# Optimization experiments

Hardware: AMD Instinct MI355X
Metric: run time of the kernel (lower is better)

## Reference

```python
import jax, jax.numpy as jnp
import numpy as np

K = 5        # spline kernel_size per dim (dim=2 -> 25 kernel weights)
NPG = 75     # MNIST superpixel nodes per graph


def _spline_conv(x, src, dst, pseudo, emask, W, root, bias):
    """SplineConv, dim=2, kernel_size=5, degree=1 open splines, aggr='mean'.
    emask in {0,1} masks out coalesced-away (duplicate/self-loop) edges."""
    n = x.shape[0]
    v = jnp.clip(pseudo, 0.0, 1.0) * (K - 1)
    bot = jnp.clip(jnp.floor(v), 0, K - 2)
    frac = v - bot                                   # [E,2]
    bot = bot.astype(jnp.int32)
    xj = x[src] * emask[:, None]                     # [E,Fin] gathered source feats
    # aggregate-then-transform: acc[k,i,:] = sum over edges into i with basis k
    acc = jnp.zeros((K * K, n, x.shape[1]), x.dtype)
    for o0 in (0, 1):
        for o1 in (0, 1):
            w = (frac[:, 0] if o0 else 1.0 - frac[:, 0]) * (frac[:, 1] if o1 else 1.0 - frac[:, 1])
            kk = (bot[:, 0] + o0) + K * (bot[:, 1] + o1)
            acc = acc.at[kk, dst].add(w[:, None] * xj)
    out = jnp.einsum('knf,kfo->no', acc, W)
    deg = jax.ops.segment_sum(emask, dst, num_segments=n)
    return out / jnp.maximum(deg, 1.0)[:, None] + x @ root + bias


def _pool(x, pos, valid, batch, src, dst, emask, size, G, B):
    """voxel_grid + max_pool with static shapes: S=B*G*G clusters, masked."""
    S = B * G * G
    c = jnp.clip(jnp.floor(pos / size).astype(jnp.int32), 0, G - 1)
    cl = batch * (G * G) + c[:, 1] * G + c[:, 0]
    xm = jnp.where(valid[:, None] > 0, x, -1e30)
    px = jax.ops.segment_max(xm, cl, num_segments=S)
    cnt = jax.ops.segment_sum(valid, cl, num_segments=S)
    sval = (cnt > 0).astype(x.dtype)
    px = jnp.where(sval[:, None] > 0, px, 0.0)
    ppos = jax.ops.segment_sum(pos * valid[:, None], cl, num_segments=S) / jnp.maximum(cnt, 1.0)[:, None]
    nb = jnp.arange(S, dtype=jnp.int32) // (G * G)
    # remap edges to clusters; mask self loops and duplicates (= coalesce)
    nsrc, ndst = cl[src], cl[dst]
    m = (emask > 0) & (nsrc != ndst)
    a0 = jnp.where(m, nsrc, S)
    b0 = jnp.where(m, ndst, S)
    order = jnp.lexsort((b0, a0))
    a, b = a0[order], b0[order]
    first = jnp.concatenate([jnp.array([True]), (a[1:] != a[:-1]) | (b[1:] != b[:-1])])
    keep = jnp.zeros(src.shape[0], dtype=bool).at[order].set(first & (a < S))
    kf = keep.astype(x.dtype)
    # T.Cartesian(cat=False, norm=True): pseudo = (pos_src-pos_dst)/(2*max|.|)+0.5
    cart = ppos[nsrc] - ppos[ndst]
    amax = jnp.maximum(jnp.max(jnp.abs(cart) * kf[:, None]), 1e-12)
    pseudo = cart / (2.0 * amax) + 0.5
    return px, ppos, sval, nb, nsrc, ndst, kf, pseudo


def _forward(x, pos, src, dst, W1, r1, b1, W2, r2, b2, W3, r3, b3, fw1, fb1, fw2, fb2):
    N = x.shape[0]
    B = N // NPG
    batch = jnp.arange(N, dtype=jnp.int32) // NPG
    valid = jnp.ones((N,), x.dtype)
    emask = jnp.ones((src.shape[0],), x.dtype)
    cart = pos[src] - pos[dst]
    pseudo = cart / (2.0 * jnp.maximum(jnp.max(jnp.abs(cart)), 1e-12)) + 0.5
    x = jax.nn.elu(_spline_conv(x, src, dst, pseudo, emask, W1, r1, b1))
    x, pos, valid, batch, src, dst, emask, pseudo = _pool(x, pos, valid, batch, src, dst, emask, 5.0, 6, B)
    x = jax.nn.elu(_spline_conv(x, src, dst, pseudo, emask, W2, r2, b2))
    x, pos, valid, batch, src, dst, emask, pseudo = _pool(x, pos, valid, batch, src, dst, emask, 7.0, 5, B)
    x = jax.nn.elu(_spline_conv(x, src, dst, pseudo, emask, W3, r3, b3))
    # max_pool_x(cluster, x, batch, size=4): 2x2 voxel grid (size=14, end=27.99)
    c = jnp.clip(jnp.floor(pos / 14.0).astype(jnp.int32), 0, 1)
    cl = batch * 4 + c[:, 1] * 2 + c[:, 0]
    xm = jnp.where(valid[:, None] > 0, x, -1e30)
    px = jax.ops.segment_max(xm, cl, num_segments=B * 4)
    cnt = jax.ops.segment_sum(valid, cl, num_segments=B * 4)
    px = jnp.where((cnt > 0)[:, None], px, 0.0)
    h = jax.nn.elu(px.reshape(B, 4 * 64) @ fw1.T + fb1)
    logits = h @ fw2.T + fb2  # F.dropout is identity in eval mode
    return jax.nn.log_softmax(logits, axis=1)


def setup_inputs() -> dict:
    key = jax.random.key(0)
    ks = jax.random.split(key, 16)
    B, EPG = 1024, 1392
    N = B * NPG
    x = jax.random.normal(ks[0], (N, 1), jnp.float32)
    pos = jax.random.uniform(ks[1], (N, 2), jnp.float32) * 27.99
    s = jax.random.randint(ks[2], (B, EPG), 0, NPG)
    d = (s + 1 + jax.random.randint(ks[3], (B, EPG), 0, NPG - 1)) % NPG  # no self loops
    off = (jnp.arange(B, dtype=jnp.int32) * NPG)[:, None]
    src = (s + off).reshape(-1)
    dst = (d + off).reshape(-1)
    rn = lambda k, sh, sc: jax.random.normal(k, sh, jnp.float32) * sc
    return dict(x=x, pos=pos, src=src, dst=dst,
                W1=rn(ks[4], (25, 1, 32), 0.2), r1=rn(ks[5], (1, 32), 0.2), b1=jnp.zeros((32,), jnp.float32),
                W2=rn(ks[6], (25, 32, 64), 0.05), r2=rn(ks[7], (32, 64), 0.1), b2=jnp.zeros((64,), jnp.float32),
                W3=rn(ks[8], (25, 64, 64), 0.04), r3=rn(ks[9], (64, 64), 0.08), b3=jnp.zeros((64,), jnp.float32),
                fw1=rn(ks[10], (128, 256), 0.06), fb1=jnp.zeros((128,), jnp.float32),
                fw2=rn(ks[11], (10, 128), 0.09), fb2=jnp.zeros((10,), jnp.float32))


def reference(x, pos, src, dst, W1, r1, b1, W2, r2, b2, W3, r3, b3, fw1, fb1, fw2, fb2):
    return _forward(x, pos, src, dst, W1, r1, b1, W2, r2, b2, W3, r3, b3, fw1, fb1, fw2, fb2)
```

## Files before the change

kernel.cpp:

```cpp
#include <hip/hip_runtime.h>
#include <math.h>

#define NPG 75
#define KDIM 5

typedef _Float16 half8 __attribute__((ext_vector_type(8)));
typedef float f32x4 __attribute__((ext_vector_type(4)));

__device__ __forceinline__ float eluf(float v){ return v > 0.f ? v : expf(v) - 1.f; }

__device__ __forceinline__ void atomAddF(float* p, float v){ unsafeAtomicAdd(p, v); }

__device__ __forceinline__ unsigned fenc(float f){
    unsigned u = __float_as_uint(f);
    return (u & 0x80000000u) ? ~u : (u | 0x80000000u);
}
__device__ __forceinline__ float fdec(unsigned u){
    return (u & 0x80000000u) ? __uint_as_float(u & 0x7FFFFFFFu) : __uint_as_float(~u);
}

__device__ __forceinline__ void fma25(float (&r)[25], const float (&wx)[5], const float (&wyx)[5]){
    #pragma unroll
    for (int b1 = 0; b1 < 5; b1++)
        #pragma unroll
        for (int b0 = 0; b0 < 5; b0++)
            asm("v_fmac_f32 %0, %1, %2" : "+v"(r[b1 * 5 + b0]) : "v"(wx[b0]), "v"(wyx[b1]));
}

__device__ __forceinline__ void spline2(float c0, float c1, float am, int* kks, float* wsp){
    float denom = 2.f * fmaxf(am, 1e-12f);
    float p0 = c0 / denom + 0.5f;
    float p1 = c1 / denom + 0.5f;
    p0 = fminf(fmaxf(p0, 0.f), 1.f) * 4.f;
    p1 = fminf(fmaxf(p1, 0.f), 1.f) * 4.f;
    float b0 = fminf(floorf(p0), 3.f);
    float b1 = fminf(floorf(p1), 3.f);
    float f0 = p0 - b0, f1 = p1 - b1;
    int i0 = (int)b0, i1 = (int)b1;
    wsp[0] = (1.f - f0) * (1.f - f1); kks[0] = i0     + KDIM *  i1;
    wsp[1] =        f0  * (1.f - f1); kks[1] = i0 + 1 + KDIM *  i1;
    wsp[2] = (1.f - f0) *        f1 ; kks[2] = i0     + KDIM * (i1 + 1);
    wsp[3] =        f0  *        f1 ; kks[3] = i0 + 1 + KDIM * (i1 + 1);
}

__device__ __forceinline__ void spline_pay(float2 c, float denom, float* d){
    float p0 = fminf(fmaxf(c.x / denom + 0.5f, 0.f), 1.f) * 4.f;
    float p1 = fminf(fmaxf(c.y / denom + 0.5f, 0.f), 1.f) * 4.f;
    float b0 = fminf(floorf(p0), 3.f);
    float b1 = fminf(floorf(p1), 3.f);
    int i0 = (int)b0, i1 = (int)b1;
    float f0 = p0 - b0, f1 = p1 - b1;
    #pragma unroll
    for (int k = 0; k < 4; k++){
        d[k]     = (k == i0) ? (1.f - f0) : ((k == i0 + 1) ? f0 : 0.f);
        d[4 + k] = (k == i1) ? (1.f - f1) : ((k == i1 + 1) ? f1 : 0.f);
    }
}

__global__ __launch_bounds__(256) void prep_k(
        const float* __restrict__ W2, const float* __restrict__ r2,
        const float* __restrict__ W3, const float* __restrict__ r3,
        _Float16* __restrict__ Wz2, _Float16* __restrict__ Wz3, int nW,
        const float* __restrict__ pos, const int* __restrict__ src,
        const int* __restrict__ dst, int E4, int gA, unsigned* __restrict__ outbits){
    const int blk = blockIdx.x;
    if (blk < nW){
        int gid = blk * 256 + threadIdx.x;
        const int T2 = 26 * 32 * 64;
        const int T3 = 26 * 64 * 64;
        const float* W; const float* root; _Float16* Wz; int FIN; int g;
        if (gid < T2){ W = W2; root = r2; Wz = Wz2; FIN = 32; g = gid; }
        else if (gid < T2 + T3){ W = W3; root = r3; Wz = Wz3; FIN = 64; g = gid - T2; }
        else return;
        int k = g >> 6, n = g & 63;
        float v = (k < 25 * FIN) ? W[(size_t)k * 64 + n] : root[(size_t)(k - 25 * FIN) * 64 + n];
        int kt = k >> 5, kr = k & 31, quad = kr >> 3, j = kr & 7;
        int lane = (quad << 4) | (n & 15);
        int nt = n >> 4;
        Wz[(((size_t)(kt * 4 + nt) * 64 + lane) << 3) + j] = (_Float16)v;
    } else {
        float cand = 0.f;
        for (int i = (blk - nW) * 256 + threadIdx.x; i < E4; i += gA * 256){
            int4 s4 = ((const int4*)src)[i];
            int4 d4 = ((const int4*)dst)[i];
            #pragma unroll
            for (int k = 0; k < 4; k++){
                int s = (&s4.x)[k], d = (&d4.x)[k];
                float c0 = pos[s*2]   - pos[d*2];
                float c1 = pos[s*2+1] - pos[d*2+1];
                cand = fmaxf(cand, fmaxf(fabsf(c0), fabsf(c1)));
            }
        }
        __shared__ float sm[256];
        sm[threadIdx.x] = cand; __syncthreads();
        for (int o = 128; o > 0; o >>= 1){
            if (threadIdx.x < o) sm[threadIdx.x] = fmaxf(sm[threadIdx.x], sm[threadIdx.x + o]);
            __syncthreads();
        }
        if (threadIdx.x == 0) atomicMax(outbits, __float_as_uint(sm[0]));
    }
}

__global__ __launch_bounds__(512) void conv1dedup_k(
        const float* __restrict__ x, const float* __restrict__ pos,
        const int* __restrict__ src, const int* __restrict__ dst, int EPG,
        const unsigned* __restrict__ amaxp,
        const float* __restrict__ W1, const float* __restrict__ r1, const float* __restrict__ b1,
        float* __restrict__ px1, float* __restrict__ pp1, float* __restrict__ sv1,
        int* __restrict__ easrc, float2* __restrict__ ecart,
        int* __restrict__ rowptr2, int* __restrict__ kcnt, unsigned* __restrict__ amaxbits){
    __shared__ __align__(16) float acc[NPG * 28];
    __shared__ float deg[NPG];
    __shared__ float xl[NPG], p0l[NPG], p1l[NPG];
    __shared__ int   cli[NPG];
    __shared__ float W1s[800], r1s[32], b1s[32];
    __shared__ unsigned px[36 * 32];
    __shared__ float cnt[36], ps[72], ppS[72];
    __shared__ unsigned pm[36 * 36];
    __shared__ float degs[36];
    __shared__ int rs[37], cur[36];
    __shared__ float red[8];
    __shared__ unsigned short sdS[2048];

    const int b = blockIdx.x, t = threadIdx.x;
    const int lane = t & 63, wid = t >> 6;
    const int n0 = b * NPG, e0 = b * EPG;

    const float am = __uint_as_float(*amaxp);

    for (int i = t; i < NPG * 28; i += 512) acc[i] = 0.f;
    for (int i = t; i < 36 * 32; i += 512) px[i] = 0u;
    for (int i = t; i < 36 * 36; i += 512) pm[i] = 0xFFFFFFFFu;
    if (t < NPG) deg[t] = 0.f;
    if (t < 36){ cnt[t] = 0.f; degs[t] = 0.f; }
    if (t < 72) ps[t] = 0.f;
    for (int i = t; i < 800; i += 512) W1s[i] = W1[i];
    if (t < 32){ r1s[t] = r1[t]; b1s[t] = b1[t]; }
    if (t < NPG){
        float p0 = pos[(n0 + t) * 2], p1 = pos[(n0 + t) * 2 + 1];
        xl[t] = x[n0 + t]; p0l[t] = p0; p1l[t] = p1;
        int c0 = min(max((int)floorf(p0 / 5.f), 0), 5);
        int c1 = min(max((int)floorf(p1 / 5.f), 0), 5);
        cli[t] = c1 * 6 + c0;
    }
    __syncthreads();

    if (t < NPG){
        int c = cli[t];
        atomAddF(&cnt[c], 1.f);
        atomAddF(&ps[c*2],     p0l[t]);
        atomAddF(&ps[c*2 + 1], p1l[t]);
    }
    #pragma unroll 4
    for (int it = 0; it < 4; it++){
        int e = t + it * 512;
        if (e < EPG){
            int s = src[e0 + e] - n0;
            int d = dst[e0 + e] - n0;
            sdS[e] = (unsigned short)(s | (d << 8));
            float c0 = p0l[s] - p0l[d];
            float c1 = p1l[s] - p1l[d];
            int kks[4]; float wsp[4];
            spline2(c0, c1, am, kks, wsp);
            float xv = xl[s];
            #pragma unroll
            for (int c = 0; c < 4; c++) atomAddF(&acc[d*28 + kks[c]], wsp[c] * xv);
            atomAddF(&deg[d], 1.f);
        }
    }
    __syncthreads();

    if (t < 36){
        float c = cnt[t], m = fmaxf(c, 1.f);
        float q0 = ps[t*2] / m, q1 = ps[t*2 + 1] / m;
        ppS[t*2] = q0; ppS[t*2 + 1] = q1;
        pp1[(b*36 + t)*2]     = q0;
        pp1[(b*36 + t)*2 + 1] = q1;
        sv1[b*36 + t] = (c > 0.f) ? 1.f : 0.f;
    }
    {
        const int o = t & 31;
        float wreg[25];
        #pragma unroll
        for (int k = 0; k < 25; k++) wreg[k] = W1s[k * 32 + o];
        const float rro = r1s[o], bbo = b1s[o];
        const int ii = t >> 5;
        #pragma unroll
        for (int r = 0; r < 5; r++){
            int i = ii + r * 16;
            if (i < NPG){
                const float4* ar = (const float4*)(acc + i * 28);
                float s = 0.f;
                #pragma unroll
                for (int q = 0; q < 7; q++){
                    float4 aq = ar[q];
                    s += aq.x * wreg[q*4];
                    if (q*4 + 1 < 25) s += aq.y * wreg[q*4 + 1];
                    if (q*4 + 2 < 25) s += aq.z * wreg[q*4 + 2];
                    if (q*4 + 3 < 25) s += aq.w * wreg[q*4 + 3];
                }
                float v = s / fmaxf(deg[i], 1.f) + xl[i] * rro + bbo;
                v = eluf(v);
                atomicMax(&px[cli[i]*32 + o], fenc(v));
            }
        }
    }
    int lab[4];
    #pragma unroll 4
    for (int it = 0; it < 4; it++){
        int e = t + it * 512;
        lab[it] = 0;
        if (e < EPG){
            int sd = (int)sdS[e];
            int a  = cli[sd & 255];
            int bb = cli[sd >> 8];
            lab[it] = a | (bb << 8) | ((a != bb) ? 0x10000 : 0);
            if (a != bb) atomicMin(&pm[a * 36 + bb], (unsigned)e);
        }
    }
    __syncthreads();

    for (int idx = t; idx < 36 * 32; idx += 512){
        int s_ = idx >> 5;
        px1[(size_t)(b*36)*32 + idx] = (cnt[s_] > 0.f) ? fdec(px[idx]) : 0.f;
    }
    float cand = 0.f;
    unsigned keptM = 0;
    #pragma unroll 4
    for (int it = 0; it < 4; it++){
        int e = t + it * 512;
        int L = lab[it];
        if (L & 0x10000){
            int a = L & 255, bb = (L >> 8) & 255;
            if (pm[a * 36 + bb] == (unsigned)e){
                keptM |= 1u << it;
                atomAddF(&degs[bb], 1.f);
                float c0 = ppS[a*2]     - ppS[bb*2];
                float c1 = ppS[a*2 + 1] - ppS[bb*2 + 1];
                cand = fmaxf(cand, fmaxf(fabsf(c0), fabsf(c1)));
            }
        }
    }
    #pragma unroll
    for (int o = 1; o < 64; o <<= 1) cand = fmaxf(cand, __shfl_xor(cand, o, 64));
    if (lane == 0) red[wid] = cand;
    __syncthreads();
    if (t == 0){
        float m = red[0];
        #pragma unroll
        for (int i = 1; i < 8; i++) m = fmaxf(m, red[i]);
        atomicMax(amaxbits, __float_as_uint(m));
    }
    if (t < 64){
        int v = (t < 36) ? (int)degs[t] : 0;
        int incl = v;
        #pragma unroll
        for (int o = 1; o < 64; o <<= 1){
            int u = __shfl_up(incl, o, 64);
            if (t >= o) incl += u;
        }
        if (t == 0) rs[0] = 0;
        if (t < 36) rs[t + 1] = incl;
    }
    __syncthreads();
    if (t < 36){
        rowptr2[(b*36 + t)*2]     = e0 + rs[t];
        rowptr2[(b*36 + t)*2 + 1] = e0 + rs[t + 1];
        cur[t] = rs[t];
    }
    if (t == 0) kcnt[b] = rs[36];
    __syncthreads();
    #pragma unroll 4
    for (int it = 0; it < 4; it++){
        if (keptM & (1u << it)){
            int L = lab[it];
            int a = L & 255, bb = (L >> 8) & 255;
            int slot = atomicAdd(&cur[bb], 1);
            easrc[e0 + slot] = b*36 + a;
            ecart[e0 + slot] = make_float2(ppS[a*2] - ppS[bb*2], ppS[a*2 + 1] - ppS[bb*2 + 1]);
        }
    }
}

__global__ __launch_bounds__(1024) void dedup_pool_k(
        const int* __restrict__ easrc_in, const int* __restrict__ rowptr_in,
        const int* __restrict__ kcnt_in,
        const float* __restrict__ xin,
        const float* __restrict__ pp1, const float* __restrict__ sv1,
        int EPG,
        float* __restrict__ px2, float* __restrict__ pp2, float* __restrict__ sv2,
        int* __restrict__ easrc, float2* __restrict__ ecart,
        int* __restrict__ rowptr2, int* __restrict__ kcnt, unsigned* __restrict__ amaxbits){
    constexpr int GG = 25, NN = 36;
    __shared__ unsigned pm[GG * GG];
    __shared__ float degs[GG];
    __shared__ int rs[GG + 1];
    __shared__ int cur[GG];
    __shared__ float red[16];
    __shared__ int   clS[NN];
    __shared__ int   vld[NN];
    __shared__ int   rsS[NN + 1];
    __shared__ float ppS[2 * GG];
    __shared__ unsigned px[GG * 64];
    __shared__ float cnt[GG], ps[2 * GG];
    __shared__ unsigned short abS[1280];

    const int b = blockIdx.x, t = threadIdx.x;
    const int lane = t & 63, wid = t >> 6;
    const int e0 = b * EPG;
    const int cb25 = b * GG;
    const int nb36 = b * NN;

    for (int i = t; i < GG * GG; i += 1024) pm[i] = 0xFFFFFFFFu;
    for (int i = t; i < GG * 64; i += 1024) px[i] = 0u;
    if (t < GG){ degs[t] = 0.f; cnt[t] = 0.f; }
    if (t < 2 * GG) ps[t] = 0.f;
    if (t < NN){
        float v  = sv1[nb36 + t];
        float p0 = pp1[(nb36 + t)*2], p1 = pp1[(nb36 + t)*2 + 1];
        int c0 = min(max((int)floorf(p0 / 7.f), 0), 4);
        int c1 = min(max((int)floorf(p1 / 7.f), 0), 4);
        clS[t] = c1 * 5 + c0;
        vld[t] = (v > 0.f) ? 1 : 0;
        rsS[t] = rowptr_in[(nb36 + t)*2] - e0;
    }
    if (t == 0) rsS[NN] = kcnt_in[b];
    __syncthreads();

    const int kn = rsS[NN];

    if (t < NN && vld[t]){
        int c = clS[t];
        atomAddF(&cnt[c], 1.f);
        atomAddF(&ps[c*2],     pp1[(nb36 + t)*2]);
        atomAddF(&ps[c*2 + 1], pp1[(nb36 + t)*2 + 1]);
    }
    for (int idx = t; idx < NN * 64; idx += 1024){
        int i = idx >> 6, f = idx & 63;
        if (vld[i])
            atomicMax(&px[clS[i]*64 + f], fenc(xin[(size_t)(nb36 + i)*64 + f]));
    }
    #pragma unroll 2
    for (int it = 0; it < 2; it++){
        int s = t + it * 1024;
        if (s < kn){
            int r = 0;
            while (r < NN - 1 && rsS[r + 1] <= s) r++;
            int a2 = clS[easrc_in[e0 + s] - nb36];
            int b2 = clS[r];
            abS[s] = (unsigned short)(a2 | (b2 << 8) | ((a2 != b2) ? 0x8000 : 0));
            if (a2 != b2) atomicMin(&pm[a2 * GG + b2], (unsigned)s);
        }
    }
    __syncthreads();

    if (t < GG){
        float c = cnt[t], m = fmaxf(c, 1.f);
        float q0 = ps[t*2] / m, q1 = ps[t*2 + 1] / m;
        ppS[t*2] = q0; ppS[t*2 + 1] = q1;
        pp2[(cb25 + t)*2]     = q0;
        pp2[(cb25 + t)*2 + 1] = q1;
        sv2[cb25 + t] = (c > 0.f) ? 1.f : 0.f;
    }
    for (int idx = t; idx < GG * 64; idx += 1024){
        int s_ = idx >> 6;
        px2[(size_t)cb25*64 + idx] = (cnt[s_] > 0.f) ? fdec(px[idx]) : 0.f;
    }
    __syncthreads();

    float cand = 0.f;
    #pragma unroll 2
    for (int it = 0; it < 2; it++){
        int s = t + it * 1024;
        if (s < kn){
            int A = (int)abS[s];
            if (A & 0x8000){
                int a2 = A & 255, b2 = (A >> 8) & 127;
                if (pm[a2 * GG + b2] == (unsigned)s){
                    atomAddF(&degs[b2], 1.f);
                    float c0 = ppS[a2*2]     - ppS[b2*2];
                    float c1 = ppS[a2*2 + 1] - ppS[b2*2 + 1];
                    cand = fmaxf(cand, fmaxf(fabsf(c0), fabsf(c1)));
                }
            }
        }
    }
    #pragma unroll
    for (int o = 1; o < 64; o <<= 1) cand = fmaxf(cand, __shfl_xor(cand, o, 64));
    if (lane == 0) red[wid] = cand;
    __syncthreads();
    if (t == 0){
        float m = red[0];
        #pragma unroll
        for (int i = 1; i < 16; i++) m = fmaxf(m, red[i]);
        atomicMax(amaxbits, __float_as_uint(m));
    }
    if (t < 64){
        int v = (t < GG) ? (int)degs[t] : 0;
        int incl = v;
        #pragma unroll
        for (int o = 1; o < 64; o <<= 1){
            int u = __shfl_up(incl, o, 64);
            if (t >= o) incl += u;
        }
        if (t == 0) rs[0] = 0;
        if (t < GG) rs[t + 1] = incl;
    }
    __syncthreads();
    if (t < GG){
        rowptr2[(cb25 + t)*2]     = e0 + rs[t];
        rowptr2[(cb25 + t)*2 + 1] = e0 + rs[t + 1];
        cur[t] = rs[t];
    }
    if (t == 0) kcnt[b] = rs[GG];
    __syncthreads();
    #pragma unroll 2
    for (int it = 0; it < 2; it++){
        int s = t + it * 1024;
        if (s < kn){
            int A = (int)abS[s];
            if (A & 0x8000){
                int a2 = A & 255, b2 = (A >> 8) & 127;
                if (pm[a2 * GG + b2] == (unsigned)s){
                    int slot = atomicAdd(&cur[b2], 1);
                    easrc[e0 + slot] = cb25 + a2;
                    ecart[e0 + slot] = make_float2(ppS[a2*2] - ppS[b2*2], ppS[a2*2 + 1] - ppS[b2*2 + 1]);
                }
            }
        }
    }
}

__global__ __launch_bounds__(256) void conv_gather32_k(
        const float* __restrict__ x, const int* __restrict__ easrc,
        const float2* __restrict__ ecart, const unsigned* __restrict__ amaxp,
        const int* __restrict__ rowptr2, _Float16* __restrict__ Aout){
    constexpr int FIN = 32;
    constexpr int KTOT = 26 * FIN;
    __shared__ __align__(16) float pay[4][36][8];
    __shared__ int asrcS[4][36];
    const int w = threadIdx.x >> 6, lane = threadIdx.x & 63;
    const int node = blockIdx.x * 4 + w;
    const int row0 = rowptr2[node*2], row1 = rowptr2[node*2 + 1];
    const int ne = row1 - row0;
    const int sub = lane >> 5;
    const int f = lane & (FIN - 1);

    if (lane < ne){
        float am = __uint_as_float(*amaxp);
        spline_pay(ecart[row0 + lane], 2.f * fmaxf(am, 1e-12f), &pay[w][lane][0]);
        asrcS[w][lane] = easrc[row0 + lane];
    }

    float r[25];
    #pragma unroll
    for (int b = 0; b < 25; b++) r[b] = 0.f;

    int j = sub;
    int aNext = 0;
    float xvCur = 0.f;
    if (j < ne){
        int aCur = asrcS[w][j];
        xvCur = x[(size_t)aCur * FIN + f];
        int j1 = (j + 2 < ne) ? j + 2 : j;
        aNext = asrcS[w][j1];
    }
    for (; j < ne; j += 2){
        int jN  = j + 2;
        int jNs = (jN < ne) ? jN : j;
        int jN2 = (jN + 2 < ne) ? jN + 2 : jNs;
        float xvN = x[(size_t)aNext * FIN + f];
        int aN2 = asrcS[w][jN2];
        float4 wa = *(const float4*)&pay[w][j][0];
        float4 wb = *(const float4*)&pay[w][j][4];
        float wx4 = 1.f - (wa.x + wa.y + wa.z + wa.w);
        float wy4 = 1.f - (wb.x + wb.y + wb.z + wb.w);
        float wx[5]  = {wa.x, wa.y, wa.z, wa.w, wx4};
        float wyx[5] = {wb.x * xvCur, wb.y * xvCur, wb.z * xvCur, wb.w * xvCur, wy4 * xvCur};
        fma25(r, wx, wyx);
        xvCur = xvN; aNext = aN2;
    }

    #pragma unroll
    for (int b = 0; b < 25; b++) r[b] += __shfl_xor(r[b], 32, 64);

    float inv = 1.f / (float)max(ne, 1);
    _Float16* dstrow = Aout + (size_t)node * KTOT;
    #pragma unroll
    for (int b = 0; b < 25; b++)
        if ((b & 1) == sub) dstrow[b * 32 + f] = (_Float16)(r[b] * inv);
    if (sub == 0) dstrow[25 * 32 + f] = (_Float16)x[(size_t)node * 32 + f];
}

__global__ __launch_bounds__(256) void conv_mfma832_k(
        const _Float16* __restrict__ A, const _Float16* __restrict__ Wz,
        const float* __restrict__ bias, int M, float* __restrict__ out){
    constexpr int KTOT = 832;
    constexpr int NSTEP = KTOT / 32;
    const int w = threadIdx.x >> 6, lane = threadIdx.x & 63;
    const int m0 = blockIdx.x * 64 + w * 16;
    const int quad = lane >> 4;

    f32x4 acc[4];
    #pragma unroll
    for (int nt = 0; nt < 4; nt++) acc[nt] = (f32x4){0.f, 0.f, 0.f, 0.f};

    const half8* __restrict__ Arow = (const half8*)(A + (size_t)(m0 + (lane & 15)) * KTOT);
    const half8* __restrict__ Wp   = (const half8*)Wz + lane;

    for (int kt = 0; kt < NSTEP; kt++){
        half8 a = Arow[kt * 4 + quad];
        #pragma unroll
        for (int nt = 0; nt < 4; nt++){
            half8 b = Wp[(kt * 4 + nt) * 64];
            acc[nt] = __builtin_amdgcn_mfma_f32_16x16x32_f16(a, b, acc[nt], 0, 0, 0);
        }
    }

    float* cp = out + (size_t)m0 * 64;
    const int r = quad * 4, c = lane & 15;
    #pragma unroll
    for (int nt = 0; nt < 4; nt++){
        float bv = bias[nt * 16 + c];
        #pragma unroll
        for (int i = 0; i < 4; i++)
            cp[(size_t)(r + i) * 64 + nt * 16 + c] = eluf(acc[nt][i] + bv);
    }
}

__global__ __launch_bounds__(1024) void conv3pf_k(
        const float* __restrict__ x,
        const int* __restrict__ easrc, const float2* __restrict__ ecart,
        const unsigned* __restrict__ amaxp,
        const int* __restrict__ rowptr3,
        const _Float16* __restrict__ Wz, const float* __restrict__ bias,
        const float* __restrict__ pp2, const float* __restrict__ sv2,
        const float* __restrict__ fw1, const float* __restrict__ fb1,
        const float* __restrict__ fw2, const float* __restrict__ fb2,
        float* __restrict__ out){
    constexpr int PAD = 1672;
    __shared__ __align__(16) _Float16 Alds[32 * PAD];
    __shared__ __align__(16) float scr[4096];
    __shared__ int asrcS[16][24];
    __shared__ unsigned px4[4 * 64];
    __shared__ float cnt4[4];
    __shared__ int cli25[25];
    __shared__ float xr[256];
    __shared__ float h[128];
    __shared__ float lg[10];
    __shared__ float lse;

    const int b = blockIdx.x, t = threadIdx.x;
    const int w = t >> 6, lane = t & 63;
    const int cb25 = b * 25;

    {
        unsigned* az = (unsigned*)&Alds[25 * PAD];
        for (int i = t; i < 7 * PAD / 2; i += 1024) az[i] = 0u;
    }
    if (t < 256) px4[t] = 0u;
    if (t < 4) cnt4[t] = 0.f;
    if (t < 25){
        float v = sv2[cb25 + t];
        float p0 = pp2[(cb25 + t)*2], p1 = pp2[(cb25 + t)*2 + 1];
        int c0 = min(max((int)floorf(p0 / 14.f), 0), 1);
        int c1 = min(max((int)floorf(p1 / 14.f), 0), 1);
        cli25[t] = (v > 0.f) ? (c1 * 2 + c0) : -1;
    }

    const float am = __uint_as_float(*amaxp);
    const float denom = 2.f * fmaxf(am, 1e-12f);
    float* payW = scr + w * 192;

    #pragma unroll
    for (int i = 0; i < 2; i++){
        const int nloc = w * 2 + i;
        if (nloc < 25){
            const int node = cb25 + nloc;
            const int row0 = rowptr3[node*2], row1 = rowptr3[node*2 + 1];
            const int ne = row1 - row0;

            if (lane < ne){
                spline_pay(ecart[row0 + lane], denom, payW + lane * 8);
                asrcS[w][lane] = easrc[row0 + lane];
            }

            float r[25];
            #pragma unroll
            for (int bq = 0; bq < 25; bq++) r[bq] = 0.f;

            int j = 0;
            int aNext = 0;
            float xvCur = 0.f;
            if (j < ne){
                int aCur = asrcS[w][j];
                xvCur = x[(size_t)aCur * 64 + lane];
                int j1 = (1 < ne) ? 1 : 0;
                aNext = asrcS[w][j1];
            }
            for (; j < ne; j++){
                int jN  = j + 1;
                int jNs = (jN < ne) ? jN : j;
                int jN2 = (jN + 1 < ne) ? jN + 1 : jNs;
                float xvN = x[(size_t)aNext * 64 + lane];
                int aN2 = asrcS[w][jN2];
                float4 wa = *(const float4*)(payW + j * 8);
                float4 wb = *(const float4*)(payW + j * 8 + 4);
                float wx4 = 1.f - (wa.x + wa.y + wa.z + wa.w);
                float wy4 = 1.f - (wb.x + wb.y + wb.z + wb.w);
                float wx[5]  = {wa.x, wa.y, wa.z, wa.w, wx4};
                float wyx[5] = {wb.x * xvCur, wb.y * xvCur, wb.z * xvCur, wb.w * xvCur, wy4 * xvCur};
                fma25(r, wx, wyx);
                xvCur = xvN; aNext = aN2;
            }

            float inv = 1.f / (float)max(ne, 1);
            _Float16* dstrow = &Alds[nloc * PAD];
            #pragma unroll
            for (int bq = 0; bq < 25; bq++) dstrow[bq * 64 + lane] = (_Float16)(r[bq] * inv);
            dstrow[25 * 64 + lane] = (_Float16)x[(size_t)node * 64 + lane];
        }
    }
    __syncthreads();

    if (t < 25 && cli25[t] >= 0) atomAddF(&cnt4[cli25[t]], 1.f);

    float* Cpart = scr;
    float* out3L = scr + 2048;

    const int tile = w & 7, khalf = w >> 3;
    const int mt = tile >> 2, nt = tile & 3;
    const int quad = lane >> 4, mr = lane & 15;
    f32x4 acc = (f32x4){0.f, 0.f, 0.f, 0.f};
    const _Float16* arow = &Alds[(mt * 16 + mr) * PAD];
    const half8* __restrict__ Wp = (const half8*)Wz + lane;
    const int kt0 = khalf * 26;
    for (int kt = 0; kt < 26; kt++){
        half8 a = *(const half8*)(arow + (kt0 + kt) * 32 + quad * 8);
        half8 bb = Wp[((kt0 + kt) * 4 + nt) * 64];
        acc = __builtin_amdgcn_mfma_f32_16x16x32_f16(a, bb, acc, 0, 0, 0);
    }
    const int r_ = quad * 4, c_ = lane & 15;
    if (khalf == 1){
        float* Cp = Cpart + tile * 256;
        #pragma unroll
        for (int i = 0; i < 4; i++) Cp[(r_ + i) * 16 + c_] = acc[i];
    }
    __syncthreads();
    if (khalf == 0){
        const float* Cp = Cpart + tile * 256;
        float bv = bias[nt * 16 + c_];
        #pragma unroll
        for (int i = 0; i < 4; i++)
            out3L[(mt * 16 + r_ + i) * 64 + nt * 16 + c_] = eluf(acc[i] + Cp[(r_ + i) * 16 + c_] + bv);
    }
    __syncthreads();

    for (int idx = t; idx < 25 * 64; idx += 1024){
        int i = idx >> 6, f = idx & 63;
        if (cli25[i] >= 0)
            atomicMax(&px4[cli25[i]*64 + f], fenc(out3L[i * 64 + f]));
    }
    __syncthreads();
    if (t < 256) xr[t] = (cnt4[t >> 6] > 0.f) ? fdec(px4[t]) : 0.f;
    __syncthreads();
    if (t < 128){
        float s = fb1[t];
        const float4* wrow = (const float4*)(fw1 + (size_t)t * 256);
        #pragma unroll 4
        for (int i = 0; i < 64; i++){
            float4 q = wrow[i];
            s += xr[i*4]   * q.x;
            s += xr[i*4+1] * q.y;
            s += xr[i*4+2] * q.z;
            s += xr[i*4+3] * q.w;
        }
        h[t] = eluf(s);
    }
    __syncthreads();
    if (t < 10){
        float s2 = fb2[t];
        const float* w2 = fw2 + (size_t)t * 128;
        for (int j = 0; j < 128; j++) s2 += h[j] * w2[j];
        lg[t] = s2;
    }
    __syncthreads();
    if (t == 0){
        float m = lg[0];
        for (int c = 1; c < 10; c++) m = fmaxf(m, lg[c]);
        float se = 0.f;
        for (int c = 0; c < 10; c++) se += expf(lg[c] - m);
        lse = m + logf(se);
    }
    __syncthreads();
    if (t < 10) out[(size_t)b*10 + t] = lg[t] - lse;
}

extern "C" void kernel_launch(void* const* d_in, const int* in_sizes, int n_in,
                              void* d_out, int out_size, void* d_ws, size_t ws_size,
                              hipStream_t stream) {
    const float* x   = (const float*)d_in[0];
    const float* pos = (const float*)d_in[1];
    const int*   src = (const int*)d_in[2];
    const int*   dst = (const int*)d_in[3];
    const float* W1  = (const float*)d_in[4];
    const float* r1  = (const float*)d_in[5];
    const float* b1  = (const float*)d_in[6];
    const float* W2  = (const float*)d_in[7];
    const float* r2  = (const float*)d_in[8];
    const float* b2  = (const float*)d_in[9];
    const float* W3  = (const float*)d_in[10];
    const float* r3  = (const float*)d_in[11];
    const float* b3  = (const float*)d_in[12];
    const float* fw1 = (const float*)d_in[13];
    const float* fb1 = (const float*)d_in[14];
    const float* fw2 = (const float*)d_in[15];
    const float* fb2 = (const float*)d_in[16];
    float* out = (float*)d_out;

    const int N   = in_sizes[0];
    const int E   = in_sizes[2];
    const int B   = N / NPG;
    const int EPG = E / B;
    const int S1  = B * 36;
    const int S2  = B * 25;

    float* w = (float*)d_ws;
    size_t off = 0;
    auto alloc = [&](size_t nelem){ size_t o = off; off += (nelem + 63) & ~(size_t)63; return o; };

    size_t o_scal = alloc(4);
    size_t o_px1  = alloc((size_t)S1 * 32);
    size_t o_pp1  = alloc((size_t)S1 * 2);
    size_t o_sv1  = alloc(S1);
    size_t o_easrc= alloc(E);
    size_t o_ecart= alloc((size_t)2 * E);
    size_t o_kcnt = alloc(B);
    size_t o_rp2  = alloc((size_t)2 * S1);
    size_t o_rp3  = alloc((size_t)2 * S2);
    size_t o_out2 = alloc((size_t)S1 * 64);
    size_t o_px2  = alloc((size_t)S2 * 64);
    size_t o_pp2  = alloc((size_t)S2 * 2);
    size_t o_sv2  = alloc(S2);
    size_t o_wz2  = alloc((size_t)26 * 32 * 64 / 2 + 64);
    size_t o_wz3  = alloc((size_t)26 * 64 * 64 / 2 + 64);
    size_t o_accA = alloc(((size_t)S1 * 832 + 1) / 2);

    hipMemsetAsync(w + o_scal, 0, 4 * sizeof(float), stream);

    unsigned* scal = (unsigned*)(w + o_scal);
    _Float16* Wz2  = (_Float16*)(w + o_wz2);
    _Float16* Wz3  = (_Float16*)(w + o_wz3);
    _Float16* A16  = (_Float16*)(w + o_accA);

    const int E4 = E / 4;
    int gA = (E4 + 255) / 256; if (gA > 512) gA = 512;
    const int nW = (26 * 32 * 64 + 26 * 64 * 64 + 255) / 256;
    prep_k<<<nW + gA, 256, 0, stream>>>(W2, r2, W3, r3, Wz2, Wz3, nW,
                                        pos, src, dst, E4, gA, scal + 0);

    conv1dedup_k<<<B, 512, 0, stream>>>(x, pos, src, dst, EPG, scal + 0, W1, r1, b1,
                                        w + o_px1, w + o_pp1, w + o_sv1,
                                        (int*)(w + o_easrc), (float2*)(w + o_ecart),
                                        (int*)(w + o_rp2), (int*)(w + o_kcnt), scal + 1);

    conv_gather32_k<<<S1 / 4, 256, 0, stream>>>(
        w + o_px1, (int*)(w + o_easrc), (const float2*)(w + o_ecart), scal + 1,
        (int*)(w + o_rp2), A16);
    conv_mfma832_k<<<S1 / 64, 256, 0, stream>>>(A16, Wz2, b2, S1, w + o_out2);

    dedup_pool_k<<<B, 1024, 0, stream>>>(
        (int*)(w + o_easrc), (int*)(w + o_rp2), (int*)(w + o_kcnt),
        w + o_out2, w + o_pp1, w + o_sv1, EPG,
        w + o_px2, w + o_pp2, w + o_sv2,
        (int*)(w + o_easrc), (float2*)(w + o_ecart),
        (int*)(w + o_rp3), (int*)(w + o_kcnt), scal + 2);

    conv3pf_k<<<B, 1024, 0, stream>>>(
        w + o_px2,
        (int*)(w + o_easrc), (const float2*)(w + o_ecart), scal + 2,
        (int*)(w + o_rp3), Wz3, b3,
        w + o_pp2, w + o_sv2,
        fw1, fb1, fw2, fb2, out);
}
```

Baseline: 320.1 us.

## Fuse conv2 MFMA GEMM into per-graph dedup/pool kernel, dropping out2 buffer

Merges the conv2 MFMA GEMM into the dedup/voxel-pool kernel, giving one 256-thread block per graph. Each graph's 36 cluster rows are multiplied in 16-row tiles, and the ELU output is max-reduced straight into shared pooled features through atomicMax, so the out2 intermediate is never written to or read from global memory. This removes a kernel launch and the global round trip. In exchange, the dedup block shrinks from 1024 to 256 threads and some MFMA work is wasted on padded rows (36 rows spread over 48), which may lower parallelism per graph.

```diff
diff --git a/kernel.cpp b/kernel.cpp
--- a/kernel.cpp
+++ b/kernel.cpp
@@ -282,155 +282,6 @@
     }
 }
 
-__global__ __launch_bounds__(1024) void dedup_pool_k(
-        const int* __restrict__ easrc_in, const int* __restrict__ rowptr_in,
-        const int* __restrict__ kcnt_in,
-        const float* __restrict__ xin,
-        const float* __restrict__ pp1, const float* __restrict__ sv1,
-        int EPG,
-        float* __restrict__ px2, float* __restrict__ pp2, float* __restrict__ sv2,
-        int* __restrict__ easrc, float2* __restrict__ ecart,
-        int* __restrict__ rowptr2, int* __restrict__ kcnt, unsigned* __restrict__ amaxbits){
-    constexpr int GG = 25, NN = 36;
-    __shared__ unsigned pm[GG * GG];
-    __shared__ float degs[GG];
-    __shared__ int rs[GG + 1];
-    __shared__ int cur[GG];
-    __shared__ float red[16];
-    __shared__ int   clS[NN];
-    __shared__ int   vld[NN];
-    __shared__ int   rsS[NN + 1];
-    __shared__ float ppS[2 * GG];
-    __shared__ unsigned px[GG * 64];
-    __shared__ float cnt[GG], ps[2 * GG];
-    __shared__ unsigned short abS[1280];
-
-    const int b = blockIdx.x, t = threadIdx.x;
-    const int lane = t & 63, wid = t >> 6;
-    const int e0 = b * EPG;
-    const int cb25 = b * GG;
-    const int nb36 = b * NN;
-
-    for (int i = t; i < GG * GG; i += 1024) pm[i] = 0xFFFFFFFFu;
-    for (int i = t; i < GG * 64; i += 1024) px[i] = 0u;
-    if (t < GG){ degs[t] = 0.f; cnt[t] = 0.f; }
-    if (t < 2 * GG) ps[t] = 0.f;
-    if (t < NN){
-        float v  = sv1[nb36 + t];
-        float p0 = pp1[(nb36 + t)*2], p1 = pp1[(nb36 + t)*2 + 1];
-        int c0 = min(max((int)floorf(p0 / 7.f), 0), 4);
-        int c1 = min(max((int)floorf(p1 / 7.f), 0), 4);
-        clS[t] = c1 * 5 + c0;
-        vld[t] = (v > 0.f) ? 1 : 0;
-        rsS[t] = rowptr_in[(nb36 + t)*2] - e0;
-    }
-    if (t == 0) rsS[NN] = kcnt_in[b];
-    __syncthreads();
-
-    const int kn = rsS[NN];
-
-    if (t < NN && vld[t]){
-        int c = clS[t];
-        atomAddF(&cnt[c], 1.f);
-        atomAddF(&ps[c*2],     pp1[(nb36 + t)*2]);
-        atomAddF(&ps[c*2 + 1], pp1[(nb36 + t)*2 + 1]);
-    }
-    for (int idx = t; idx < NN * 64; idx += 1024){
-        int i = idx >> 6, f = idx & 63;
-        if (vld[i])
-            atomicMax(&px[clS[i]*64 + f], fenc(xin[(size_t)(nb36 + i)*64 + f]));
-    }
-    #pragma unroll 2
-    for (int it = 0; it < 2; it++){
-        int s = t + it * 1024;
-        if (s < kn){
-            int r = 0;
-            while (r < NN - 1 && rsS[r + 1] <= s) r++;
-            int a2 = clS[easrc_in[e0 + s] - nb36];
-            int b2 = clS[r];
-            abS[s] = (unsigned short)(a2 | (b2 << 8) | ((a2 != b2) ? 0x8000 : 0));
-            if (a2 != b2) atomicMin(&pm[a2 * GG + b2], (unsigned)s);
-        }
-    }
-    __syncthreads();
-
-    if (t < GG){
-        float c = cnt[t], m = fmaxf(c, 1.f);
-        float q0 = ps[t*2] / m, q1 = ps[t*2 + 1] / m;
-        ppS[t*2] = q0; ppS[t*2 + 1] = q1;
-        pp2[(cb25 + t)*2]     = q0;
-        pp2[(cb25 + t)*2 + 1] = q1;
-        sv2[cb25 + t] = (c > 0.f) ? 1.f : 0.f;
-    }
-    for (int idx = t; idx < GG * 64; idx += 1024){
-        int s_ = idx >> 6;
-        px2[(size_t)cb25*64 + idx] = (cnt[s_] > 0.f) ? fdec(px[idx]) : 0.f;
-    }
-    __syncthreads();
-
-    float cand = 0.f;
-    #pragma unroll 2
-    for (int it = 0; it < 2; it++){
-        int s = t + it * 1024;
-        if (s < kn){
-            int A = (int)abS[s];
-            if (A & 0x8000){
-                int a2 = A & 255, b2 = (A >> 8) & 127;
-                if (pm[a2 * GG + b2] == (unsigned)s){
-                    atomAddF(&degs[b2], 1.f);
-                    float c0 = ppS[a2*2]     - ppS[b2*2];
-                    float c1 = ppS[a2*2 + 1] - ppS[b2*2 + 1];
-                    cand = fmaxf(cand, fmaxf(fabsf(c0), fabsf(c1)));
-                }
-            }
-        }
-    }
-    #pragma unroll
-    for (int o = 1; o < 64; o <<= 1) cand = fmaxf(cand, __shfl_xor(cand, o, 64));
-    if (lane == 0) red[wid] = cand;
-    __syncthreads();
-    if (t == 0){
-        float m = red[0];
-        #pragma unroll
-        for (int i = 1; i < 16; i++) m = fmaxf(m, red[i]);
-        atomicMax(amaxbits, __float_as_uint(m));
-    }
-    if (t < 64){
-        int v = (t < GG) ? (int)degs[t] : 0;
-        int incl = v;
-        #pragma unroll
-        for (int o = 1; o < 64; o <<= 1){
-            int u = __shfl_up(incl, o, 64);
-            if (t >= o) incl += u;
-        }
-        if (t == 0) rs[0] = 0;
-        if (t < GG) rs[t + 1] = incl;
-    }
-    __syncthreads();
-    if (t < GG){
-        rowptr2[(cb25 + t)*2]     = e0 + rs[t];
-        rowptr2[(cb25 + t)*2 + 1] = e0 + rs[t + 1];
-        cur[t] = rs[t];
-    }
-    if (t == 0) kcnt[b] = rs[GG];
-    __syncthreads();
-    #pragma unroll 2
-    for (int it = 0; it < 2; it++){
-        int s = t + it * 1024;
-        if (s < kn){
-            int A = (int)abS[s];
-            if (A & 0x8000){
-                int a2 = A & 255, b2 = (A >> 8) & 127;
-                if (pm[a2 * GG + b2] == (unsigned)s){
-                    int slot = atomicAdd(&cur[b2], 1);
-                    easrc[e0 + slot] = cb25 + a2;
-                    ecart[e0 + slot] = make_float2(ppS[a2*2] - ppS[b2*2], ppS[a2*2 + 1] - ppS[b2*2 + 1]);
-                }
-            }
-        }
-    }
-}
-
 __global__ __launch_bounds__(256) void conv_gather32_k(
         const float* __restrict__ x, const int* __restrict__ easrc,
         const float2* __restrict__ ecart, const unsigned* __restrict__ amaxp,
@@ -492,39 +343,176 @@
     if (sub == 0) dstrow[25 * 32 + f] = (_Float16)x[(size_t)node * 32 + f];
 }
 
-__global__ __launch_bounds__(256) void conv_mfma832_k(
+__global__ __launch_bounds__(256) void mfma2pool_k(
         const _Float16* __restrict__ A, const _Float16* __restrict__ Wz,
-        const float* __restrict__ bias, int M, float* __restrict__ out){
-    constexpr int KTOT = 832;
-    constexpr int NSTEP = KTOT / 32;
-    const int w = threadIdx.x >> 6, lane = threadIdx.x & 63;
-    const int m0 = blockIdx.x * 64 + w * 16;
-    const int quad = lane >> 4;
-
-    f32x4 acc[4];
+        const float* __restrict__ bias,
+        const int* __restrict__ easrc_in, const int* __restrict__ rowptr_in,
+        const int* __restrict__ kcnt_in,
+        const float* __restrict__ pp1, const float* __restrict__ sv1,
+        int EPG,
+        float* __restrict__ px2, float* __restrict__ pp2, float* __restrict__ sv2,
+        int* __restrict__ easrc, float2* __restrict__ ecart,
+        int* __restrict__ rowptr3, int* __restrict__ kcnt, unsigned* __restrict__ amaxbits){
+    constexpr int GG = 25, NN = 36;
+    __shared__ unsigned pm[GG * GG];
+    __shared__ float degs[GG];
+    __shared__ int rs[GG + 1];
+    __shared__ int cur[GG];
+    __shared__ float red[4];
+    __shared__ int   clS[NN];
+    __shared__ int   vld[NN];
+    __shared__ int   rsS[NN + 1];
+    __shared__ float ppS[2 * GG];
+    __shared__ unsigned px[GG * 64];
+    __shared__ float cnt[GG], ps[2 * GG];
+    __shared__ unsigned short abS[1280];
+
+    const int b = blockIdx.x, t = threadIdx.x;
+    const int w = t >> 6, lane = t & 63;
+    const int e0 = b * EPG;
+    const int cb25 = b * GG;
+    const int nb36 = b * NN;
+
+    for (int i = t; i < GG * GG; i += 256) pm[i] = 0xFFFFFFFFu;
+    for (int i = t; i < GG * 64; i += 256) px[i] = 0u;
+    if (t < GG){ degs[t] = 0.f; cnt[t] = 0.f; }
+    if (t < 2 * GG) ps[t] = 0.f;
+    if (t < NN){
+        float v  = sv1[nb36 + t];
+        float p0 = pp1[(nb36 + t)*2], p1 = pp1[(nb36 + t)*2 + 1];
+        int c0 = min(max((int)floorf(p0 / 7.f), 0), 4);
+        int c1 = min(max((int)floorf(p1 / 7.f), 0), 4);
+        clS[t] = c1 * 5 + c0;
+        vld[t] = (v > 0.f) ? 1 : 0;
+        rsS[t] = rowptr_in[(nb36 + t)*2] - e0;
+    }
+    if (t == 0) rsS[NN] = kcnt_in[b];
+    __syncthreads();
+
+    const int kn = rsS[NN];
+
+    if (t < NN && vld[t]){
+        int c = clS[t];
+        atomAddF(&cnt[c], 1.f);
+        atomAddF(&ps[c*2],     pp1[(nb36 + t)*2]);
+        atomAddF(&ps[c*2 + 1], pp1[(nb36 + t)*2 + 1]);
+    }
+    #pragma unroll 6
+    for (int it = 0; it < 6; it++){
+        int s = t + it * 256;
+        if (s < kn){
+            int r = 0;
+            while (r < NN - 1 && rsS[r + 1] <= s) r++;
+            int a2 = clS[easrc_in[e0 + s] - nb36];
+            int b2 = clS[r];
+            abS[s] = (unsigned short)(a2 | (b2 << 8) | ((a2 != b2) ? 0x8000 : 0));
+            if (a2 != b2) atomicMin(&pm[a2 * GG + b2], (unsigned)s);
+        }
+    }
+    {
+        const int quad = lane >> 4, c_ = lane & 15;
+        const half8* __restrict__ Wp = (const half8*)Wz + lane;
+        #pragma unroll
+        for (int tt = 0; tt < 3; tt++){
+            const int tile = w + tt * 4;
+            const int mt = tile >> 2, nt = tile & 3;
+            const int row_l = mt * 16 + c_;
+            const bool rok = (row_l < NN);
+            const half8* Arow = rok ? (const half8*)(A + (size_t)(nb36 + row_l) * 832) : (const half8*)A;
+            f32x4 acc = (f32x4){0.f, 0.f, 0.f, 0.f};
+            for (int kt = 0; kt < 26; kt++){
+                half8 a = rok ? Arow[kt * 4 + quad] : (half8){};
+                half8 bb = Wp[(kt * 4 + nt) * 64];
+                acc = __builtin_amdgcn_mfma_f32_16x16x32_f16(a, bb, acc, 0, 0, 0);
+            }
+            const int r_ = quad * 4;
+            float bv = bias[nt * 16 + c_];
+            #pragma unroll
+            for (int i = 0; i < 4; i++){
+                int rowp = mt * 16 + r_ + i;
+                if (rowp < NN && vld[rowp]){
+                    float v = eluf(acc[i] + bv);
+                    atomicMax(&px[clS[rowp]*64 + nt * 16 + c_], fenc(v));
+                }
+            }
+        }
+    }
+    __syncthreads();
+
+    if (t < GG){
+        float c = cnt[t], m = fmaxf(c, 1.f);
+        float q0 = ps[t*2] / m, q1 = ps[t*2 + 1] / m;
+        ppS[t*2] = q0; ppS[t*2 + 1] = q1;
+        pp2[(cb25 + t)*2]     = q0;
+        pp2[(cb25 + t)*2 + 1] = q1;
+        sv2[cb25 + t] = (c > 0.f) ? 1.f : 0.f;
+    }
+    for (int idx = t; idx < GG * 64; idx += 256){
+        int s_ = idx >> 6;
+        px2[(size_t)cb25*64 + idx] = (cnt[s_] > 0.f) ? fdec(px[idx]) : 0.f;
+    }
+    __syncthreads();
+
+    float cand = 0.f;
+    #pragma unroll 6
+    for (int it = 0; it < 6; it++){
+        int s = t + it * 256;
+        if (s < kn){
+            int A_ = (int)abS[s];
+            if (A_ & 0x8000){
+                int a2 = A_ & 255, b2 = (A_ >> 8) & 127;
+                if (pm[a2 * GG + b2] == (unsigned)s){
+                    atomAddF(&degs[b2], 1.f);
+                    float c0 = ppS[a2*2]     - ppS[b2*2];
+                    float c1 = ppS[a2*2 + 1] - ppS[b2*2 + 1];
+                    cand = fmaxf(cand, fmaxf(fabsf(c0), fabsf(c1)));
+                }
+            }
+        }
+    }
     #pragma unroll
-    for (int nt = 0; nt < 4; nt++) acc[nt] = (f32x4){0.f, 0.f, 0.f, 0.f};
-
-    const half8* __restrict__ Arow = (const half8*)(A + (size_t)(m0 + (lane & 15)) * KTOT);
-    const half8* __restrict__ Wp   = (const half8*)Wz + lane;
-
-    for (int kt = 0; kt < NSTEP; kt++){
-        half8 a = Arow[kt * 4 + quad];
-        #pragma unroll
-        for (int nt = 0; nt < 4; nt++){
-            half8 b = Wp[(kt * 4 + nt) * 64];
-            acc[nt] = __builtin_amdgcn_mfma_f32_16x16x32_f16(a, b, acc[nt], 0, 0, 0);
-        }
-    }
-
-    float* cp = out + (size_t)m0 * 64;
-    const int r = quad * 4, c = lane & 15;
-    #pragma unroll
-    for (int nt = 0; nt < 4; nt++){
-        float bv = bias[nt * 16 + c];
-        #pragma unroll
-        for (int i = 0; i < 4; i++)
-            cp[(size_t)(r + i) * 64 + nt * 16 + c] = eluf(acc[nt][i] + bv);
+    for (int o = 1; o < 64; o <<= 1) cand = fmaxf(cand, __shfl_xor(cand, o, 64));
+    if (lane == 0) red[w] = cand;
+    __syncthreads();
+    if (t == 0){
+        float m = red[0];
+        #pragma unroll
+        for (int i = 1; i < 4; i++) m = fmaxf(m, red[i]);
+        atomicMax(amaxbits, __float_as_uint(m));
+    }
+    if (t < 64){
+        int v = (t < GG) ? (int)degs[t] : 0;
+        int incl = v;
+        #pragma unroll
+        for (int o = 1; o < 64; o <<= 1){
+            int u = __shfl_up(incl, o, 64);
+            if (t >= o) incl += u;
+        }
+        if (t == 0) rs[0] = 0;
+        if (t < GG) rs[t + 1] = incl;
+    }
+    __syncthreads();
+    if (t < GG){
+        rowptr3[(cb25 + t)*2]     = e0 + rs[t];
+        rowptr3[(cb25 + t)*2 + 1] = e0 + rs[t + 1];
+        cur[t] = rs[t];
+    }
+    if (t == 0) kcnt[b] = rs[GG];
+    __syncthreads();
+    #pragma unroll 6
+    for (int it = 0; it < 6; it++){
+        int s = t + it * 256;
+        if (s < kn){
+            int A_ = (int)abS[s];
+            if (A_ & 0x8000){
+                int a2 = A_ & 255, b2 = (A_ >> 8) & 127;
+                if (pm[a2 * GG + b2] == (unsigned)s){
+                    int slot = atomicAdd(&cur[b2], 1);
+                    easrc[e0 + slot] = cb25 + a2;
+                    ecart[e0 + slot] = make_float2(ppS[a2*2] - ppS[b2*2], ppS[a2*2 + 1] - ppS[b2*2 + 1]);
+                }
+            }
+        }
     }
 }
 
@@ -738,13 +726,12 @@
     size_t o_kcnt = alloc(B);
     size_t o_rp2  = alloc((size_t)2 * S1);
     size_t o_rp3  = alloc((size_t)2 * S2);
-    size_t o_out2 = alloc((size_t)S1 * 64);
     size_t o_px2  = alloc((size_t)S2 * 64);
     size_t o_pp2  = alloc((size_t)S2 * 2);
     size_t o_sv2  = alloc(S2);
     size_t o_wz2  = alloc((size_t)26 * 32 * 64 / 2 + 64);
     size_t o_wz3  = alloc((size_t)26 * 64 * 64 / 2 + 64);
-    size_t o_accA = alloc(((size_t)S1 * 832 + 1) / 2);
+    size_t o_accA = alloc(((size_t)S1 * 832 + 1) / 2 + 64);
 
     hipMemsetAsync(w + o_scal, 0, 4 * sizeof(float), stream);
 
@@ -767,11 +754,11 @@
     conv_gather32_k<<<S1 / 4, 256, 0, stream>>>(
         w + o_px1, (int*)(w + o_easrc), (const float2*)(w + o_ecart), scal + 1,
         (int*)(w + o_rp2), A16);
-    conv_mfma832_k<<<S1 / 64, 256, 0, stream>>>(A16, Wz2, b2, S1, w + o_out2);
-
-    dedup_pool_k<<<B, 1024, 0, stream>>>(
+
+    mfma2pool_k<<<B, 256, 0, stream>>>(
+        A16, Wz2, b2,
         (int*)(w + o_easrc), (int*)(w + o_rp2), (int*)(w + o_kcnt),
-        w + o_out2, w + o_pp1, w + o_sv1, EPG,
+        w + o_pp1, w + o_sv1, EPG,
         w + o_px2, w + o_pp2, w + o_sv2,
         (int*)(w + o_easrc), (float2*)(w + o_ecart),
         (int*)(w + o_rp3), (int*)(w + o_kcnt), scal + 2);
```

After: 349.2 us. 1.09x slower.

## Split conv3 fused kernel into separate gather and MFMA+head kernels

Applied to the files above, without the earlier changes.

The fused per-graph conv3 kernel, which gathered spline-weighted neighbor features into a large LDS tile before running MFMA, is split in two. A gather kernel now processes four nodes per 256-thread block and writes the fp16 A matrix to global memory. A second 1024-thread kernel reads A rows straight from global for the MFMA, then does pooling and the FC head. This frees the large LDS allocation and spreads the gather across many small blocks, at the cost of an extra launch and a global round trip for A.

```diff
diff --git a/kernel.cpp b/kernel.cpp
--- a/kernel.cpp
+++ b/kernel.cpp
@@ -528,20 +528,69 @@
     }
 }
 
-__global__ __launch_bounds__(1024) void conv3pf_k(
-        const float* __restrict__ x,
-        const int* __restrict__ easrc, const float2* __restrict__ ecart,
-        const unsigned* __restrict__ amaxp,
-        const int* __restrict__ rowptr3,
+__global__ __launch_bounds__(256) void conv_gather64_k(
+        const float* __restrict__ x, const int* __restrict__ easrc,
+        const float2* __restrict__ ecart, const unsigned* __restrict__ amaxp,
+        const int* __restrict__ rowptr2, _Float16* __restrict__ Aout){
+    constexpr int KTOT = 1664;
+    __shared__ __align__(16) float pay[4][36][8];
+    __shared__ int asrcS[4][36];
+    const int w = threadIdx.x >> 6, lane = threadIdx.x & 63;
+    const int node = blockIdx.x * 4 + w;
+    const int row0 = rowptr2[node*2], row1 = rowptr2[node*2 + 1];
+    const int ne = row1 - row0;
+
+    if (lane < ne){
+        float am = __uint_as_float(*amaxp);
+        spline_pay(ecart[row0 + lane], 2.f * fmaxf(am, 1e-12f), &pay[w][lane][0]);
+        asrcS[w][lane] = easrc[row0 + lane];
+    }
+
+    float r[25];
+    #pragma unroll
+    for (int b = 0; b < 25; b++) r[b] = 0.f;
+
+    int j = 0;
+    int aNext = 0;
+    float xvCur = 0.f;
+    if (j < ne){
+        int aCur = asrcS[w][j];
+        xvCur = x[(size_t)aCur * 64 + lane];
+        int j1 = (1 < ne) ? 1 : 0;
+        aNext = asrcS[w][j1];
+    }
+    for (; j < ne; j++){
+        int jN  = j + 1;
+        int jNs = (jN < ne) ? jN : j;
+        int jN2 = (jN + 1 < ne) ? jN + 1 : jNs;
+        float xvN = x[(size_t)aNext * 64 + lane];
+        int aN2 = asrcS[w][jN2];
+        float4 wa = *(const float4*)&pay[w][j][0];
+        float4 wb = *(const float4*)&pay[w][j][4];
+        float wx4 = 1.f - (wa.x + wa.y + wa.z + wa.w);
+        float wy4 = 1.f - (wb.x + wb.y + wb.z + wb.w);
+        float wx[5]  = {wa.x, wa.y, wa.z, wa.w, wx4};
+        float wyx[5] = {wb.x * xvCur, wb.y * xvCur, wb.z * xvCur, wb.w * xvCur, wy4 * xvCur};
+        fma25(r, wx, wyx);
+        xvCur = xvN; aNext = aN2;
+    }
+
+    float inv = 1.f / (float)max(ne, 1);
+    _Float16* dstrow = Aout + (size_t)node * KTOT;
+    #pragma unroll
+    for (int b = 0; b < 25; b++) dstrow[b * 64 + lane] = (_Float16)(r[b] * inv);
+    dstrow[25 * 64 + lane] = (_Float16)x[(size_t)node * 64 + lane];
+}
+
+__global__ __launch_bounds__(1024) void mfma3final_k(
+        const _Float16* __restrict__ A,
         const _Float16* __restrict__ Wz, const float* __restrict__ bias,
         const float* __restrict__ pp2, const float* __restrict__ sv2,
         const float* __restrict__ fw1, const float* __restrict__ fb1,
         const float* __restrict__ fw2, const float* __restrict__ fb2,
         float* __restrict__ out){
-    constexpr int PAD = 1672;
-    __shared__ __align__(16) _Float16 Alds[32 * PAD];
-    __shared__ __align__(16) float scr[4096];
-    __shared__ int asrcS[16][24];
+    __shared__ __align__(16) float Cpart[8 * 256];
+    __shared__ __align__(16) float out3L[32 * 64];
     __shared__ unsigned px4[4 * 64];
     __shared__ float cnt4[4];
     __shared__ int cli25[25];
@@ -554,10 +603,6 @@
     const int w = t >> 6, lane = t & 63;
     const int cb25 = b * 25;
 
-    {
-        unsigned* az = (unsigned*)&Alds[25 * PAD];
-        for (int i = t; i < 7 * PAD / 2; i += 1024) az[i] = 0u;
-    }
     if (t < 256) px4[t] = 0u;
     if (t < 4) cnt4[t] = 0.f;
     if (t < 25){
@@ -567,80 +612,24 @@
         int c1 = min(max((int)floorf(p1 / 14.f), 0), 1);
         cli25[t] = (v > 0.f) ? (c1 * 2 + c0) : -1;
     }
-
-    const float am = __uint_as_float(*amaxp);
-    const float denom = 2.f * fmaxf(am, 1e-12f);
-    float* payW = scr + w * 192;
-
-    #pragma unroll
-    for (int i = 0; i < 2; i++){
-        const int nloc = w * 2 + i;
-        if (nloc < 25){
-            const int node = cb25 + nloc;
-            const int row0 = rowptr3[node*2], row1 = rowptr3[node*2 + 1];
-            const int ne = row1 - row0;
-
-            if (lane < ne){
-                spline_pay(ecart[row0 + lane], denom, payW + lane * 8);
-                asrcS[w][lane] = easrc[row0 + lane];
-            }
-
-            float r[25];
-            #pragma unroll
-            for (int bq = 0; bq < 25; bq++) r[bq] = 0.f;
-
-            int j = 0;
-            int aNext = 0;
-            float xvCur = 0.f;
-            if (j < ne){
-                int aCur = asrcS[w][j];
-                xvCur = x[(size_t)aCur * 64 + lane];
-                int j1 = (1 < ne) ? 1 : 0;
-                aNext = asrcS[w][j1];
-            }
-            for (; j < ne; j++){
-                int jN  = j + 1;
-                int jNs = (jN < ne) ? jN : j;
-                int jN2 = (jN + 1 < ne) ? jN + 1 : jNs;
-                float xvN = x[(size_t)aNext * 64 + lane];
-                int aN2 = asrcS[w][jN2];
-                float4 wa = *(const float4*)(payW + j * 8);
-                float4 wb = *(const float4*)(payW + j * 8 + 4);
-                float wx4 = 1.f - (wa.x + wa.y + wa.z + wa.w);
-                float wy4 = 1.f - (wb.x + wb.y + wb.z + wb.w);
-                float wx[5]  = {wa.x, wa.y, wa.z, wa.w, wx4};
-                float wyx[5] = {wb.x * xvCur, wb.y * xvCur, wb.z * xvCur, wb.w * xvCur, wy4 * xvCur};
-                fma25(r, wx, wyx);
-                xvCur = xvN; aNext = aN2;
-            }
-
-            float inv = 1.f / (float)max(ne, 1);
-            _Float16* dstrow = &Alds[nloc * PAD];
-            #pragma unroll
-            for (int bq = 0; bq < 25; bq++) dstrow[bq * 64 + lane] = (_Float16)(r[bq] * inv);
-            dstrow[25 * 64 + lane] = (_Float16)x[(size_t)node * 64 + lane];
-        }
-    }
-    __syncthreads();
-
+    __syncthreads();
     if (t < 25 && cli25[t] >= 0) atomAddF(&cnt4[cli25[t]], 1.f);
-
-    float* Cpart = scr;
-    float* out3L = scr + 2048;
 
     const int tile = w & 7, khalf = w >> 3;
     const int mt = tile >> 2, nt = tile & 3;
-    const int quad = lane >> 4, mr = lane & 15;
+    const int quad = lane >> 4, c_ = lane & 15;
+    const int row_l = mt * 16 + c_;
+    const int rowc = (row_l < 25) ? row_l : 24;
+    const half8* __restrict__ Arow = (const half8*)(A + (size_t)(cb25 + rowc) * 1664);
+    const half8* __restrict__ Wp = (const half8*)Wz + lane;
     f32x4 acc = (f32x4){0.f, 0.f, 0.f, 0.f};
-    const _Float16* arow = &Alds[(mt * 16 + mr) * PAD];
-    const half8* __restrict__ Wp = (const half8*)Wz + lane;
     const int kt0 = khalf * 26;
     for (int kt = 0; kt < 26; kt++){
-        half8 a = *(const half8*)(arow + (kt0 + kt) * 32 + quad * 8);
+        half8 a = Arow[(kt0 + kt) * 4 + quad];
         half8 bb = Wp[((kt0 + kt) * 4 + nt) * 64];
         acc = __builtin_amdgcn_mfma_f32_16x16x32_f16(a, bb, acc, 0, 0, 0);
     }
-    const int r_ = quad * 4, c_ = lane & 15;
+    const int r_ = quad * 4;
     if (khalf == 1){
         float* Cp = Cpart + tile * 256;
         #pragma unroll
@@ -744,7 +733,8 @@
     size_t o_sv2  = alloc(S2);
     size_t o_wz2  = alloc((size_t)26 * 32 * 64 / 2 + 64);
     size_t o_wz3  = alloc((size_t)26 * 64 * 64 / 2 + 64);
-    size_t o_accA = alloc(((size_t)S1 * 832 + 1) / 2);
+    size_t accAhalfs = (size_t)S1 * 832 > (size_t)S2 * 1664 ? (size_t)S1 * 832 : (size_t)S2 * 1664;
+    size_t o_accA = alloc((accAhalfs + 1) / 2);
 
     hipMemsetAsync(w + o_scal, 0, 4 * sizeof(float), stream);
 
@@ -776,10 +766,12 @@
         (int*)(w + o_easrc), (float2*)(w + o_ecart),
         (int*)(w + o_rp3), (int*)(w + o_kcnt), scal + 2);
 
-    conv3pf_k<<<B, 1024, 0, stream>>>(
-        w + o_px2,
-        (int*)(w + o_easrc), (const float2*)(w + o_ecart), scal + 2,
-        (int*)(w + o_rp3), Wz3, b3,
+    conv_gather64_k<<<S2 / 4, 256, 0, stream>>>(
+        w + o_px2, (int*)(w + o_easrc), (const float2*)(w + o_ecart), scal + 2,
+        (int*)(w + o_rp3), A16);
+
+    mfma3final_k<<<B, 1024, 0, stream>>>(
+        A16, Wz3, b3,
         w + o_pp2, w + o_sv2,
         fw1, fb1, fw2, fb2, out);
 }
```

New measurement: 351.7 us. 9.9% more time.
